# Optimization experiments

Measured on AMD Instinct MI355X. Metric: run time of the kernel, lower is better.

Reference implementation:

```python
import jax, jax.numpy as jnp
import numpy as np

METRIC = [1.0, 1.0, 1.0, 0.0]  # Cl(3,0,1) projective geometric algebra
N_BLADES = 1 << len(METRIC)    # 16
BATCH = 2097152


def _build_cayley(metric):
    """Cayley structure-constant tensor C[i,j,k]: (a b)_k = sum_ij a_i b_j C[i,j,k].
    Blades indexed by bitmask over generators; e_A e_B = sign * e_{A xor B}."""
    d = len(metric)
    n = 1 << d
    cay = np.zeros((n, n, n), dtype=np.float32)
    for A in range(n):
        for B in range(n):
            # canonical reordering sign (count transpositions)
            sa, s = A >> 1, 0
            while sa:
                s += bin(sa & B).count("1")
                sa >>= 1
            sign = -1.0 if (s & 1) else 1.0
            # contract common generators through the metric
            for i in range(d):
                if A & B & (1 << i):
                    sign *= metric[i]
            if sign != 0.0:
                cay[A, B, A ^ B] = sign
    return cay


def setup_inputs() -> dict:
    key = jax.random.key(0)
    k1, k2 = jax.random.split(key)
    a = jax.random.normal(k1, (BATCH, N_BLADES), dtype=jnp.float32)
    b = jax.random.normal(k2, (BATCH, N_BLADES), dtype=jnp.float32)
    cayley = jnp.asarray(_build_cayley(METRIC))  # [16,16,16], sparse structure constants
    return {"a": a, "b": b, "cayley": cayley}


def reference(a, b, cayley):
    # Geometric product: (a b)_k = sum_{i,j} a_i b_j C[i,j,k]
    a = a.astype(jnp.float32)
    b = b.astype(jnp.float32)
    return jnp.einsum("...i,ijk,...j->...k", a, cayley, b)
```

## Files before the change

### kernel.cpp

```cpp
#include <hip/hip_runtime.h>


__host__ __device__ constexpr float cayley_sign(int A, int B) {
    int s = 0;
    for (int sa = A >> 1; sa; sa >>= 1) s += __builtin_popcount(sa & B);
    float sign = (s & 1) ? -1.0f : 1.0f;
    if (A & B & 8) sign = 0.0f;
    return sign;
}

__device__ __forceinline__ int swz(int p) {
    return (p & ~3) | ((p ^ (p >> 3)) & 3);
}

typedef float vfloat4 __attribute__((ext_vector_type(4)));

__global__ void __launch_bounds__(256)
gp_cl301_kernel(const float4* __restrict__ a4,
                const float4* __restrict__ b4,
                float4* __restrict__ o4,
                int ntiles) {
    __shared__ float4 lds[4][2][256];

    const int l = threadIdx.x & 63;
    const int w = threadIdx.x >> 6;
    float4* sl_a = &lds[w][0][0];
    float4* sl_b = &lds[w][1][0];

    const int wave_id = blockIdx.x * 4 + w;
    const int nwaves  = gridDim.x * 4;

    for (int t = wave_id; t < ntiles; t += nwaves) {
        const long base = (long)t * 256;

        asm volatile("s_waitcnt lgkmcnt(0)" ::: "memory");

        #pragma unroll
        for (int q = 0; q < 4; ++q) {
            const int ps = swz(q * 64 + l);
            __builtin_amdgcn_global_load_lds(
                (const __attribute__((address_space(1))) void*)(a4 + base + ps),
                (__attribute__((address_space(3))) void*)(sl_a + q * 64),
                16, 0, 0);
            __builtin_amdgcn_global_load_lds(
                (const __attribute__((address_space(1))) void*)(b4 + base + ps),
                (__attribute__((address_space(3))) void*)(sl_b + q * 64),
                16, 0, 0);
        }
        asm volatile("s_waitcnt vmcnt(0)" ::: "memory");
        __builtin_amdgcn_sched_barrier(0);

        float A[16], B[16];
        #pragma unroll
        for (int c = 0; c < 4; ++c) {
            const int s = l * 4 + (c ^ ((l >> 1) & 3));
            const float4 va = sl_a[s];
            const float4 vb = sl_b[s];
            A[c*4+0] = va.x; A[c*4+1] = va.y; A[c*4+2] = va.z; A[c*4+3] = va.w;
            B[c*4+0] = vb.x; B[c*4+1] = vb.y; B[c*4+2] = vb.z; B[c*4+3] = vb.w;
        }

        float O[16] = {0,0,0,0, 0,0,0,0, 0,0,0,0, 0,0,0,0};
        #pragma unroll
        for (int ii = 0; ii < 16; ++ii) {
            #pragma unroll
            for (int jj = 0; jj < 16; ++jj) {
                const float s = cayley_sign(ii, jj);
                if (s != 0.0f) {
                    O[ii ^ jj] += s * A[ii] * B[jj];
                }
            }
        }

        #pragma unroll
        for (int c = 0; c < 4; ++c) {
            const int s = l * 4 + (c ^ ((l >> 1) & 3));
            sl_a[s] = make_float4(O[c*4+0], O[c*4+1], O[c*4+2], O[c*4+3]);
        }

        #pragma unroll
        for (int q = 0; q < 4; ++q) {
            const int p = q * 64 + l;
            float4 v = sl_a[swz(p)];
            __builtin_nontemporal_store(*(const vfloat4*)&v,
                                        (vfloat4*)(o4 + base + p));
        }
    }
}

extern "C" void kernel_launch(void* const* d_in, const int* in_sizes, int n_in,
                              void* d_out, int out_size, void* d_ws, size_t ws_size,
                              hipStream_t stream) {
    const float4* a4 = (const float4*)d_in[0];
    const float4* b4 = (const float4*)d_in[1];
    float4* o4 = (float4*)d_out;

    const int n      = in_sizes[0] / 16;
    const int ntiles = n / 64;

    const int grid = 2048;
    gp_cl301_kernel<<<grid, 256, 0, stream>>>(a4, b4, o4, ntiles);
}
```

Before: 62.47 us.

## Compute geometric product across quad lanes with DPP instead of LDS transpose

The LDS staging and swizzled transpose are removed. Each lane now loads one float4 chunk of a multivector directly, and the four lanes of a quad cooperate: B chunks are exchanged via DPP quad permutes, partial products are formed per chunk pair, and quad reductions pick out each lane's output chunk. This targets the LDS traffic and wait overhead in a memory-bound kernel. In exchange it does redundant arithmetic, because every round computes all four output chunks and then discards three, and it adds many DPP moves.

```diff
diff --git a/kernel.cpp b/kernel.cpp
--- a/kernel.cpp
+++ b/kernel.cpp
@@ -1,7 +1,7 @@
 #include <hip/hip_runtime.h>
 
 
-__host__ __device__ constexpr float cayley_sign(int A, int B) {
+__device__ __host__ inline constexpr float cayley_sign(int A, int B) {
     int s = 0;
     for (int sa = A >> 1; sa; sa >>= 1) s += __builtin_popcount(sa & B);
     float sign = (s & 1) ? -1.0f : 1.0f;
@@ -9,8 +9,46 @@
     return sign;
 }
 
-__device__ __forceinline__ int swz(int p) {
-    return (p & ~3) | ((p ^ (p >> 3)) & 3);
+__device__ __host__ inline constexpr float hsign(int a, int b) {
+    return ((a & 2) && (b & 1)) ? -1.0f : 1.0f;
+}
+
+template <int CTRL>
+__device__ __forceinline__ float qperm(float x) {
+    int xi = __builtin_bit_cast(int, x);
+    int r = __builtin_amdgcn_mov_dpp(xi, CTRL, 0xf, 0xf, true);
+    return __builtin_bit_cast(float, r);
+}
+template <int R>
+__device__ __forceinline__ float qxor(float x) {
+    if constexpr (R == 0) return x;
+    else if constexpr (R == 1) return qperm<0xB1>(x);
+    else if constexpr (R == 2) return qperm<0x4E>(x);
+    else return qperm<0x1B>(x);
+}
+
+template <int R>
+__device__ __forceinline__ void gp_round(const float (&A)[4], const float (&B)[4],
+                                         const float (&m)[4][4], int c, float (&O)[4]) {
+    float Bm[4];
+    #pragma unroll
+    for (int b = 0; b < 4; ++b) Bm[b] = qxor<R>(B[b]) * m[R][b];
+
+    float P[4] = {0.0f, 0.0f, 0.0f, 0.0f};
+    #pragma unroll
+    for (int a = 0; a < 4; ++a) {
+        #pragma unroll
+        for (int b = 0; b < 4; ++b) {
+            P[a ^ b] += hsign(a, b) * A[a] * Bm[b];
+        }
+    }
+
+    #pragma unroll
+    for (int d = 0; d < 4; ++d) {
+        float s1 = P[d] + qperm<0xB1>(P[d]);
+        float s2 = s1 + qperm<0x4E>(s1);
+        O[d] = (c == R) ? s2 : O[d];
+    }
 }
 
 typedef float vfloat4 __attribute__((ext_vector_type(4)));
@@ -20,70 +58,46 @@
                 const float4* __restrict__ b4,
                 float4* __restrict__ o4,
                 int ntiles) {
-    __shared__ float4 lds[4][2][256];
-
     const int l = threadIdx.x & 63;
     const int w = threadIdx.x >> 6;
-    float4* sl_a = &lds[w][0][0];
-    float4* sl_b = &lds[w][1][0];
+    const int c = l & 3;
+
+    float m[4][4];
+    #pragma unroll
+    for (int r = 0; r < 4; ++r) {
+        #pragma unroll
+        for (int b = 0; b < 4; ++b) {
+            m[r][b] = cayley_sign(4 * c, 4 * (c ^ r) + b);
+        }
+    }
 
     const int wave_id = blockIdx.x * 4 + w;
     const int nwaves  = gridDim.x * 4;
 
     for (int t = wave_id; t < ntiles; t += nwaves) {
-        const long base = (long)t * 256;
+        const long base = (long)t * 256 + l;
 
-        asm volatile("s_waitcnt lgkmcnt(0)" ::: "memory");
-
+        float4 ra[4], rb[4];
         #pragma unroll
         for (int q = 0; q < 4; ++q) {
-            const int ps = swz(q * 64 + l);
-            __builtin_amdgcn_global_load_lds(
-                (const __attribute__((address_space(1))) void*)(a4 + base + ps),
-                (__attribute__((address_space(3))) void*)(sl_a + q * 64),
-                16, 0, 0);
-            __builtin_amdgcn_global_load_lds(
-                (const __attribute__((address_space(1))) void*)(b4 + base + ps),
-                (__attribute__((address_space(3))) void*)(sl_b + q * 64),
-                16, 0, 0);
-        }
-        asm volatile("s_waitcnt vmcnt(0)" ::: "memory");
-        __builtin_amdgcn_sched_barrier(0);
-
-        float A[16], B[16];
-        #pragma unroll
-        for (int c = 0; c < 4; ++c) {
-            const int s = l * 4 + (c ^ ((l >> 1) & 3));
-            const float4 va = sl_a[s];
-            const float4 vb = sl_b[s];
-            A[c*4+0] = va.x; A[c*4+1] = va.y; A[c*4+2] = va.z; A[c*4+3] = va.w;
-            B[c*4+0] = vb.x; B[c*4+1] = vb.y; B[c*4+2] = vb.z; B[c*4+3] = vb.w;
-        }
-
-        float O[16] = {0,0,0,0, 0,0,0,0, 0,0,0,0, 0,0,0,0};
-        #pragma unroll
-        for (int ii = 0; ii < 16; ++ii) {
-            #pragma unroll
-            for (int jj = 0; jj < 16; ++jj) {
-                const float s = cayley_sign(ii, jj);
-                if (s != 0.0f) {
-                    O[ii ^ jj] += s * A[ii] * B[jj];
-                }
-            }
-        }
-
-        #pragma unroll
-        for (int c = 0; c < 4; ++c) {
-            const int s = l * 4 + (c ^ ((l >> 1) & 3));
-            sl_a[s] = make_float4(O[c*4+0], O[c*4+1], O[c*4+2], O[c*4+3]);
+            ra[q] = a4[base + q * 64];
+            rb[q] = b4[base + q * 64];
         }
 
         #pragma unroll
         for (int q = 0; q < 4; ++q) {
-            const int p = q * 64 + l;
-            float4 v = sl_a[swz(p)];
+            const float A[4] = {ra[q].x, ra[q].y, ra[q].z, ra[q].w};
+            const float B[4] = {rb[q].x, rb[q].y, rb[q].z, rb[q].w};
+            float O[4] = {0.0f, 0.0f, 0.0f, 0.0f};
+
+            gp_round<0>(A, B, m, c, O);
+            gp_round<1>(A, B, m, c, O);
+            gp_round<2>(A, B, m, c, O);
+            gp_round<3>(A, B, m, c, O);
+
+            float4 v = make_float4(O[0], O[1], O[2], O[3]);
             __builtin_nontemporal_store(*(const vfloat4*)&v,
-                                        (vfloat4*)(o4 + base + p));
+                                        (vfloat4*)(o4 + base + q * 64));
         }
     }
 }
```

Result: slower. 68.85 us (+10.2%).

## Double-buffer LDS tile loads per wave and shrink blocks to two waves

Applied to the files above, without the earlier changes.

Each wave now issues the global-to-LDS loads for its next tile into a second LDS buffer before computing the current tile. It waits with a partial vmcnt so that load latency overlaps compute and stores. Blocks drop from four waves to two, with the grid raised to at most 4096, so the total wave count stays the same. Each wave now uses twice the LDS, which can halve resident waves per CU and cut latency hiding from occupancy.

```diff
diff --git a/kernel.cpp b/kernel.cpp
--- a/kernel.cpp
+++ b/kernel.cpp
@@ -1,7 +1,7 @@
 #include <hip/hip_runtime.h>
 
 
-__host__ __device__ constexpr float cayley_sign(int A, int B) {
+__device__ __host__ inline constexpr float cayley_sign(int A, int B) {
     int s = 0;
     for (int sa = A >> 1; sa; sa >>= 1) s += __builtin_popcount(sa & B);
     float sign = (s & 1) ? -1.0f : 1.0f;
@@ -15,40 +15,57 @@
 
 typedef float vfloat4 __attribute__((ext_vector_type(4)));
 
-__global__ void __launch_bounds__(256)
+__global__ void __launch_bounds__(128)
 gp_cl301_kernel(const float4* __restrict__ a4,
                 const float4* __restrict__ b4,
                 float4* __restrict__ o4,
                 int ntiles) {
-    __shared__ float4 lds[4][2][256];
+    __shared__ float4 lds[2][2][2][256];
 
     const int l = threadIdx.x & 63;
     const int w = threadIdx.x >> 6;
-    float4* sl_a = &lds[w][0][0];
-    float4* sl_b = &lds[w][1][0];
 
-    const int wave_id = blockIdx.x * 4 + w;
-    const int nwaves  = gridDim.x * 4;
+    const int wave_id = blockIdx.x * 2 + w;
+    const int nwaves  = gridDim.x * 2;
 
-    for (int t = wave_id; t < ntiles; t += nwaves) {
-        const long base = (long)t * 256;
+    long t = wave_id;
+    if (t >= ntiles) return;
 
-        asm volatile("s_waitcnt lgkmcnt(0)" ::: "memory");
-
+    auto issue_tile = [&](int bufidx, long tt) {
+        const long gbase = tt * 256;
+        float4* sa = &lds[w][bufidx][0][0];
+        float4* sb = &lds[w][bufidx][1][0];
         #pragma unroll
         for (int q = 0; q < 4; ++q) {
             const int ps = swz(q * 64 + l);
             __builtin_amdgcn_global_load_lds(
-                (const __attribute__((address_space(1))) void*)(a4 + base + ps),
-                (__attribute__((address_space(3))) void*)(sl_a + q * 64),
+                (const __attribute__((address_space(1))) void*)(a4 + gbase + ps),
+                (__attribute__((address_space(3))) void*)(sa + q * 64),
                 16, 0, 0);
             __builtin_amdgcn_global_load_lds(
-                (const __attribute__((address_space(1))) void*)(b4 + base + ps),
-                (__attribute__((address_space(3))) void*)(sl_b + q * 64),
+                (const __attribute__((address_space(1))) void*)(b4 + gbase + ps),
+                (__attribute__((address_space(3))) void*)(sb + q * 64),
                 16, 0, 0);
         }
-        asm volatile("s_waitcnt vmcnt(0)" ::: "memory");
+    };
+
+    int buf = 0;
+    issue_tile(0, t);
+
+    for (;;) {
+        const long tn  = t + nwaves;
+        const bool last = (tn >= (long)ntiles);
+
+        if (!last) {
+            issue_tile(buf ^ 1, tn);
+            asm volatile("s_waitcnt vmcnt(8)" ::: "memory");
+        } else {
+            asm volatile("s_waitcnt vmcnt(0)" ::: "memory");
+        }
         __builtin_amdgcn_sched_barrier(0);
+
+        float4* sl_a = &lds[w][buf][0][0];
+        float4* sl_b = &lds[w][buf][1][0];
 
         float A[16], B[16];
         #pragma unroll
@@ -78,13 +95,18 @@
             sl_a[s] = make_float4(O[c*4+0], O[c*4+1], O[c*4+2], O[c*4+3]);
         }
 
+        const long obase = t * 256;
         #pragma unroll
         for (int q = 0; q < 4; ++q) {
             const int p = q * 64 + l;
             float4 v = sl_a[swz(p)];
             __builtin_nontemporal_store(*(const vfloat4*)&v,
-                                        (vfloat4*)(o4 + base + p));
+                                        (vfloat4*)(o4 + obase + p));
         }
+
+        if (last) break;
+        t = tn;
+        buf ^= 1;
     }
 }
 
@@ -98,6 +120,8 @@
     const int n      = in_sizes[0] / 16;
     const int ntiles = n / 64;
 
-    const int grid = 2048;
-    gp_cl301_kernel<<<grid, 256, 0, stream>>>(a4, b4, o4, ntiles);
+    int grid = (ntiles + 1) / 2;
+    if (grid > 4096) grid = 4096;
+
+    gp_cl301_kernel<<<grid, 128, 0, stream>>>(a4, b4, o4, ntiles);
 }
```

Result: no change. 63.47 us (+1.6%).
